# Kernel optimization log

Measured on AMD Instinct MI355X. Metric: run time of the kernel, lower is better.

## Reference

```python
import jax, jax.numpy as jnp
import numpy as np

N_NODES = 50000
N_EDGES = 600000
IN_DIM = 64
D = 128
N_LAYERS = 8
N_ETYPES = 44
N_MENTIONS = 100000
N_VARS = 20000
OUT_DIM = 100


def setup_inputs() -> dict:
    key = jax.random.key(0)
    ks = jax.random.split(key, 20)
    inp = {
        "node_labels": jax.random.normal(ks[0], (N_NODES, IN_DIM), jnp.float32),
        "edges": jax.random.randint(ks[1], (2, N_EDGES), 0, N_NODES, jnp.int32),
        "edge_labels": jax.random.randint(ks[2], (N_EDGES,), 0, N_ETYPES, jnp.int32),
        "var_gather": jax.random.randint(ks[3], (N_MENTIONS,), 0, N_NODES, jnp.int32),
        "var_scatter": jax.random.randint(ks[4], (N_MENTIONS,), 0, N_VARS, jnp.int32),
        "labels": jax.random.randint(ks[5], (N_VARS,), 0, OUT_DIM, jnp.int32),
        "num_vars": N_VARS,
    }
    s = 1.0 / np.sqrt(D)
    # node label encoder (2 layers)
    inp["enc_W0"] = jax.random.normal(ks[6], (IN_DIM, D), jnp.float32) / np.sqrt(IN_DIM)
    inp["enc_b0"] = jnp.zeros((D,), jnp.float32)
    inp["enc_W1"] = jax.random.normal(ks[7], (D, D), jnp.float32) * s
    inp["enc_b1"] = jnp.zeros((D,), jnp.float32)
    # 8 GGNN layers, stacked
    inp["edge_emb"] = jax.random.normal(ks[8], (N_LAYERS, N_ETYPES, D), jnp.float32) * s
    inp["mlp_W1"] = jax.random.normal(ks[9], (N_LAYERS, 3 * D, 2 * D), jnp.float32) / np.sqrt(3 * D)
    inp["mlp_b1"] = jnp.zeros((N_LAYERS, 2 * D), jnp.float32)
    inp["mlp_W2"] = jax.random.normal(ks[10], (N_LAYERS, 2 * D, D), jnp.float32) / np.sqrt(2 * D)
    inp["mlp_b2"] = jnp.zeros((N_LAYERS, D), jnp.float32)
    # independent type decoder (2 layers)
    inp["dec_W0"] = jax.random.normal(ks[11], (D, D), jnp.float32) * s
    inp["dec_b0"] = jnp.zeros((D,), jnp.float32)
    inp["dec_Wl"] = jax.random.normal(ks[12], (D, OUT_DIM), jnp.float32) * s
    inp["dec_bl"] = jnp.zeros((OUT_DIM,), jnp.float32)
    return inp


def reference(node_labels, edges, edge_labels, var_gather, var_scatter, labels, num_vars,
              enc_W0, enc_b0, enc_W1, enc_b1,
              edge_emb, mlp_W1, mlp_b1, mlp_W2, mlp_b2,
              dec_W0, dec_b0, dec_Wl, dec_bl):
    n_nodes = node_labels.shape[0]
    src, dst = edges[0], edges[1]  # message flows src -> dst (x_j = src, x_i = dst)

    # node label encoder
    h = node_labels @ enc_W0 + enc_b0
    h = jax.nn.relu(h) @ enc_W1 + enc_b1

    # message passing layers
    for l in range(edge_emb.shape[0]):
        ef = edge_emb[l][edge_labels]                       # [E, D]
        m = jnp.concatenate([h[dst], h[src], ef], axis=-1)  # [E, 3D]
        m = jax.nn.relu(m @ mlp_W1[l] + mlp_b1[l]) @ mlp_W2[l] + mlp_b2[l]
        h = jax.ops.segment_sum(m, dst, num_segments=n_nodes)
        h = jax.nn.gelu(h, approximate=False)  # torch nn.GELU (exact erf)

    # readout: gather variable mentions, scatter-mean into variables
    node_repr = h[var_gather]  # [M, D]
    sums = jax.ops.segment_sum(node_repr, var_scatter, num_segments=num_vars)
    counts = jax.ops.segment_sum(jnp.ones_like(var_scatter, jnp.float32), var_scatter, num_segments=num_vars)
    var_repr = sums / jnp.maximum(counts, 1.0)[:, None]

    # independent type decoder
    y = jax.nn.relu(var_repr @ dec_W0 + dec_b0)
    y = y @ dec_Wl + dec_bl
    return y
```

## Files before the change

### kernel.cpp

```cpp
#include <hip/hip_runtime.h>
#include <math.h>

#define N_NODES 50000
#define N_EDGES 600000
#define IN_DIM 64
#define DMODEL 128
#define N_LAYERS 8
#define N_ETYPES 44
#define N_MENTIONS 100000
#define N_VARS 20000
#define OUT_DIM 100

#define EPI_BIAS 0
#define EPI_BIAS_RELU 1
#define EPI_DEG_GELU 2
#define EPI_NONE 3

#define SCL  6.103515625e-05f
#define SCLI 16384.0f

typedef _Float16 f16x8 __attribute__((ext_vector_type(8)));
typedef _Float16 f16x4 __attribute__((ext_vector_type(4)));
typedef float f32x4 __attribute__((ext_vector_type(4)));

__device__ __forceinline__ float gelu_exact(float x) {
    return 0.5f * x * (1.0f + erff(x * 0.70710678118654752f));
}

__global__ void wprep(const float* __restrict__ src, _Float16* __restrict__ dhi,
                      _Float16* __restrict__ dlo, int K, int Nsrc, int Npad,
                      long srcLS, long dstLS, int cat) {
    __shared__ float sh[16][17];
    int z = blockIdx.z;
    src += (size_t)z * srcLS;
    dhi += (size_t)z * dstLS;
    dlo += (size_t)z * dstLS;
    int n0 = blockIdx.x * 16, k0 = blockIdx.y * 16;
    int tx = threadIdx.x, ty = threadIdx.y;
    int nr = n0 + tx, kr = k0 + ty;
    float v;
    if (cat) {
        int half = nr >> 8;
        int nc = nr & 255;
        v = src[(size_t)(kr + half * 128) * 256 + nc];
    } else {
        v = (nr < Nsrc) ? src[(size_t)kr * Nsrc + nr] : 0.f;
    }
    sh[ty][tx] = v;
    __syncthreads();
    float x = sh[tx][ty];
    int n = n0 + ty, k = k0 + tx;
    _Float16 hi = (_Float16)x;
    float lo = x - (float)hi;
    dhi[(size_t)n * K + k] = hi;
    dlo[(size_t)n * K + k] = (_Float16)lo;
}

template<int EPI, int ASPLIT, int OSPLIT, int MSWZ = 0, int NX = 8>
__global__ __launch_bounds__(256) void gemm3h(
        const float* __restrict__ A, const _Float16* __restrict__ Ahi,
        const _Float16* __restrict__ Alo,
        const _Float16* __restrict__ Bh, const _Float16* __restrict__ Bl,
        const float* __restrict__ bias, const int* __restrict__ deg,
        float* __restrict__ C, _Float16* __restrict__ Chi, _Float16* __restrict__ Clo,
        int M, int N, int K, int ldC) {
    __shared__ _Float16 Ah[64 * 56], Al[64 * 56], Bsh[64 * 56], Bsl[64 * 56];
    int t = threadIdx.x;
    int m0, n0;
    if (MSWZ) {
        int mpanels = (M + 63) >> 6;
        int per = (mpanels + 7) >> 3;
        int mi = blockIdx.x * per + blockIdx.y / NX;
        if (mi >= mpanels) return;
        m0 = mi * 64;
        n0 = (blockIdx.y % NX) * 64;
    } else {
        m0 = blockIdx.y * 64;
        n0 = blockIdx.x * 64;
    }
    int ar = t >> 2, ac = (t & 3) * 8;
    int btt = t & 127, br = btt >> 1, bc = (btt & 1) * 16;
    const _Float16* Bsrc = (t < 128) ? Bh : Bl;
    _Float16* Bdst = (t < 128) ? Bsh : Bsl;
    int lane = t & 63, wid = t >> 6;
    int wm = (wid >> 1) * 32, wn = (wid & 1) * 32;
    int quad = lane >> 4, l15 = lane & 15;
    f32x4 acc[2][2] = {};
    bool arow_ok = (m0 + ar) < M;
    const float* Aptr = ASPLIT ? nullptr : (A + (size_t)(m0 + ar) * K + ac);
    const _Float16* Ahp = ASPLIT ? (Ahi + (size_t)(m0 + ar) * K + ac) : nullptr;
    const _Float16* Alp = ASPLIT ? (Alo + (size_t)(m0 + ar) * K + ac) : nullptr;
    const _Float16* Bptr = Bsrc + (size_t)(n0 + br) * K + bc;

    for (int k0 = 0; k0 < K; k0 += 32) {
        f16x8 hv = {}, lv = {};
        if (ASPLIT) {
            if (arow_ok) {
                hv = *(const f16x8*)(Ahp + k0);
                lv = *(const f16x8*)(Alp + k0);
            }
        } else {
            float4 v0 = {0, 0, 0, 0}, v1 = {0, 0, 0, 0};
            if (arow_ok) {
                v0 = *(const float4*)(Aptr + k0);
                v1 = *(const float4*)(Aptr + k0 + 4);
            }
            float xs[8] = {v0.x, v0.y, v0.z, v0.w, v1.x, v1.y, v1.z, v1.w};
#pragma unroll
            for (int j = 0; j < 8; j++) {
                float s = xs[j] * SCL;
                _Float16 h = (_Float16)s;
                hv[j] = h;
                lv[j] = (_Float16)(s - (float)h);
            }
        }
        *(f16x8*)&Ah[ar * 56 + ac] = hv;
        *(f16x8*)&Al[ar * 56 + ac] = lv;
        f16x8 b0 = *(const f16x8*)(Bptr + k0);
        f16x8 b1v = *(const f16x8*)(Bptr + k0 + 8);
        *(f16x8*)&Bdst[br * 56 + bc] = b0;
        *(f16x8*)&Bdst[br * 56 + bc + 8] = b1v;
        __syncthreads();

        f16x8 afh[2], afl[2], bfh[2], bfl[2];
#pragma unroll
        for (int i = 0; i < 2; i++) {
            int am = (wm + i * 16 + l15) * 56 + quad * 8;
            afh[i] = *(const f16x8*)&Ah[am];
            afl[i] = *(const f16x8*)&Al[am];
            int bn = (wn + i * 16 + l15) * 56 + quad * 8;
            bfh[i] = *(const f16x8*)&Bsh[bn];
            bfl[i] = *(const f16x8*)&Bsl[bn];
        }
#pragma unroll
        for (int i = 0; i < 2; i++)
#pragma unroll
            for (int j = 0; j < 2; j++) {
                acc[i][j] = __builtin_amdgcn_mfma_f32_16x16x32_f16(afh[i], bfh[j], acc[i][j], 0, 0, 0);
                acc[i][j] = __builtin_amdgcn_mfma_f32_16x16x32_f16(afh[i], bfl[j], acc[i][j], 0, 0, 0);
                acc[i][j] = __builtin_amdgcn_mfma_f32_16x16x32_f16(afl[i], bfh[j], acc[i][j], 0, 0, 0);
            }
        __syncthreads();
    }

#pragma unroll
    for (int i = 0; i < 2; i++) {
        int rowb = m0 + wm + i * 16 + quad * 4;
#pragma unroll
        for (int j = 0; j < 2; j++) {
            int col = n0 + wn + j * 16 + l15;
            if (col >= N) continue;
#pragma unroll
            for (int r = 0; r < 4; r++) {
                int row = rowb + r;
                if (row >= M) continue;
                float v = acc[i][j][r] * SCLI;
                if (EPI == EPI_BIAS) { v += bias[col]; }
                else if (EPI == EPI_BIAS_RELU) { v += bias[col]; v = fmaxf(v, 0.f); }
                else if (EPI == EPI_DEG_GELU) { v += (float)deg[row] * bias[col]; v = gelu_exact(v); }
                if (OSPLIT == 0) {
                    C[(size_t)row * ldC + col] = v;
                } else if (OSPLIT == 1) {
                    float s = v * SCL;
                    _Float16 h = (_Float16)s;
                    size_t idx = (size_t)row * ldC + col;
                    Chi[idx] = h;
                    Clo[idx] = (_Float16)(s - (float)h);
                } else if (OSPLIT == 3) {
                    if (col < 256) C[(size_t)row * 256 + col] = v;
                    else Chi[(size_t)row * 256 + (col - 256)] = (_Float16)(v * SCL);
                }
            }
        }
    }
}

__global__ void count_deg(const int* __restrict__ dst, int* __restrict__ deg) {
    int e = blockIdx.x * blockDim.x + threadIdx.x;
    if (e < N_EDGES) atomicAdd(&deg[dst[e]], 1);
}

#define SCAN_B 1024
#define SCAN_NB ((N_NODES + SCAN_B - 1) / SCAN_B)

__global__ void scan_local(const int* __restrict__ deg, int* __restrict__ offs,
                           int* __restrict__ bsum, int n) {
    __shared__ int sh[SCAN_B];
    int t = threadIdx.x;
    int i = blockIdx.x * SCAN_B + t;
    int v = (i < n) ? deg[i] : 0;
    sh[t] = v;
    __syncthreads();
    for (int o = 1; o < SCAN_B; o <<= 1) {
        int u = (t >= o) ? sh[t - o] : 0;
        __syncthreads();
        sh[t] += u;
        __syncthreads();
    }
    if (i < n) offs[i] = sh[t] - v;
    if (t == SCAN_B - 1) bsum[blockIdx.x] = sh[t];
}

__global__ void scan_block(int* __restrict__ bsum, int nb) {
    __shared__ int sh[64];
    int t = threadIdx.x;
    int v = (t < nb) ? bsum[t] : 0;
    sh[t] = v;
    __syncthreads();
    for (int o = 1; o < 64; o <<= 1) {
        int u = (t >= o) ? sh[t - o] : 0;
        __syncthreads();
        sh[t] += u;
        __syncthreads();
    }
    if (t < nb) bsum[t] = sh[t] - v;
}

__global__ void scan_final(int* __restrict__ offs, const int* __restrict__ bsum,
                           int* __restrict__ cursor, int n, int total) {
    int i = blockIdx.x * SCAN_B + threadIdx.x;
    if (i < n) {
        int o = offs[i] + bsum[blockIdx.x];
        offs[i] = o;
        cursor[i] = o;
    }
    if (i == n) offs[n] = total;
}

__global__ void place_edges(const int* __restrict__ src, const int* __restrict__ dst,
                            const int* __restrict__ lab, int* __restrict__ cursor,
                            int* __restrict__ src_s, int* __restrict__ lab_s) {
    int e = blockIdx.x * blockDim.x + threadIdx.x;
    if (e < N_EDGES) {
        int pos = atomicAdd(&cursor[dst[e]], 1);
        src_s[pos] = src[e];
        lab_s[pos] = lab[e];
    }
}

__global__ void etype_proj_all(const float* __restrict__ edge_emb, const float* __restrict__ mlp_W1,
                               const float* __restrict__ mlp_b1, float* __restrict__ etp_all) {
    int et = blockIdx.x;
    int l  = blockIdx.y;
    int c = threadIdx.x;
    const float* ee = edge_emb + (size_t)l * N_ETYPES * DMODEL + (size_t)et * DMODEL;
    const float* W  = mlp_W1 + (size_t)l * 384 * 256 + (size_t)256 * 256;
    float s = mlp_b1[(size_t)l * 256 + c];
    for (int k = 0; k < DMODEL; k++)
        s += ee[k] * W[(size_t)k * 256 + c];
    etp_all[((size_t)l * N_ETYPES + et) * 256 + c] = s * SCL;
}

__global__ __launch_bounds__(256) void edge_agg(
        const float* __restrict__ HHd, const _Float16* __restrict__ HHs,
        const float* __restrict__ etp,
        const int* __restrict__ offsets, const int* __restrict__ src_s,
        const int* __restrict__ lab_s, _Float16* __restrict__ Phi,
        _Float16* __restrict__ Plo) {
    int wid = threadIdx.x >> 6, tl = threadIdx.x & 63;
    int i = blockIdx.x * 4 + wid;
    if (i >= N_NODES) return;
    int c4 = tl * 4;
    float4 hd = *(const float4*)&HHd[(size_t)i * 256 + c4];
    float hdx = hd.x * SCL, hdy = hd.y * SCL, hdz = hd.z * SCL, hdw = hd.w * SCL;
    float4 acc = {0.f, 0.f, 0.f, 0.f};
    int e0 = offsets[i], e1 = offsets[i + 1];
    int e = e0;
    for (; e + 3 < e1; e += 4) {
        int s0 = src_s[e],     l0 = lab_s[e];
        int s1 = src_s[e + 1], l1 = lab_s[e + 1];
        int s2 = src_s[e + 2], l2 = lab_s[e + 2];
        int s3 = src_s[e + 3], l3 = lab_s[e + 3];
        f16x4 hs0 = *(const f16x4*)&HHs[(size_t)s0 * 256 + c4];
        f16x4 hs1 = *(const f16x4*)&HHs[(size_t)s1 * 256 + c4];
        f16x4 hs2 = *(const f16x4*)&HHs[(size_t)s2 * 256 + c4];
        f16x4 hs3 = *(const f16x4*)&HHs[(size_t)s3 * 256 + c4];
        float4 et0 = *(const float4*)&etp[l0 * 256 + c4];
        float4 et1 = *(const float4*)&etp[l1 * 256 + c4];
        float4 et2 = *(const float4*)&etp[l2 * 256 + c4];
        float4 et3 = *(const float4*)&etp[l3 * 256 + c4];
        acc.x += fmaxf(hdx + (float)hs0[0] + et0.x, 0.f) + fmaxf(hdx + (float)hs1[0] + et1.x, 0.f)
               + fmaxf(hdx + (float)hs2[0] + et2.x, 0.f) + fmaxf(hdx + (float)hs3[0] + et3.x, 0.f);
        acc.y += fmaxf(hdy + (float)hs0[1] + et0.y, 0.f) + fmaxf(hdy + (float)hs1[1] + et1.y, 0.f)
               + fmaxf(hdy + (float)hs2[1] + et2.y, 0.f) + fmaxf(hdy + (float)hs3[1] + et3.y, 0.f);
        acc.z += fmaxf(hdz + (float)hs0[2] + et0.z, 0.f) + fmaxf(hdz + (float)hs1[2] + et1.z, 0.f)
               + fmaxf(hdz + (float)hs2[2] + et2.z, 0.f) + fmaxf(hdz + (float)hs3[2] + et3.z, 0.f);
        acc.w += fmaxf(hdw + (float)hs0[3] + et0.w, 0.f) + fmaxf(hdw + (float)hs1[3] + et1.w, 0.f)
               + fmaxf(hdw + (float)hs2[3] + et2.w, 0.f) + fmaxf(hdw + (float)hs3[3] + et3.w, 0.f);
    }
    for (; e < e1; ++e) {
        int s0 = src_s[e], l0 = lab_s[e];
        f16x4 hs0 = *(const f16x4*)&HHs[(size_t)s0 * 256 + c4];
        float4 et0 = *(const float4*)&etp[l0 * 256 + c4];
        acc.x += fmaxf(hdx + (float)hs0[0] + et0.x, 0.f);
        acc.y += fmaxf(hdy + (float)hs0[1] + et0.y, 0.f);
        acc.z += fmaxf(hdz + (float)hs0[2] + et0.z, 0.f);
        acc.w += fmaxf(hdw + (float)hs0[3] + et0.w, 0.f);
    }
    float sv[4] = {acc.x, acc.y, acc.z, acc.w};
    f16x4 ph, pl;
#pragma unroll
    for (int j = 0; j < 4; j++) {
        _Float16 h = (_Float16)sv[j];
        ph[j] = h;
        pl[j] = (_Float16)(sv[j] - (float)h);
    }
    *(f16x4*)&Phi[(size_t)i * 256 + c4] = ph;
    *(f16x4*)&Plo[(size_t)i * 256 + c4] = pl;
}

__global__ void readout_scatter(const _Float16* __restrict__ hhi, const _Float16* __restrict__ hlo,
                                const int* __restrict__ vg, const int* __restrict__ vs,
                                float* __restrict__ sums, int* __restrict__ cnt) {
    int m = blockIdx.x * 2 + (threadIdx.x >> 7);
    int c = threadIdx.x & 127;
    if (m >= N_MENTIONS) return;
    int node = vg[m];
    int v = vs[m];
    size_t idx = (size_t)node * DMODEL + c;
    float x = ((float)hhi[idx] + (float)hlo[idx]) * SCLI;
    atomicAdd(&sums[(size_t)v * DMODEL + c], x);
    if (c == 0) atomicAdd(&cnt[v], 1);
}

__global__ void divide_kernel(float* __restrict__ sums, const int* __restrict__ cnt) {
    int v = blockIdx.x;
    int c = threadIdx.x;
    float d = (float)max(cnt[v], 1);
    sums[(size_t)v * DMODEL + c] /= d;
}

extern "C" void kernel_launch(void* const* d_in, const int* in_sizes, int n_in,
                              void* d_out, int out_size, void* d_ws, size_t ws_size,
                              hipStream_t stream) {
    const float* node_labels = (const float*)d_in[0];
    const int*   edges       = (const int*)d_in[1];
    const int*   edge_labels = (const int*)d_in[2];
    const int*   var_gather  = (const int*)d_in[3];
    const int*   var_scatter = (const int*)d_in[4];
    const float* enc_W0 = (const float*)d_in[7];
    const float* enc_b0 = (const float*)d_in[8];
    const float* enc_W1 = (const float*)d_in[9];
    const float* enc_b1 = (const float*)d_in[10];
    const float* edge_emb = (const float*)d_in[11];
    const float* mlp_W1 = (const float*)d_in[12];
    const float* mlp_b1 = (const float*)d_in[13];
    const float* mlp_W2 = (const float*)d_in[14];
    const float* mlp_b2 = (const float*)d_in[15];
    const float* dec_W0 = (const float*)d_in[16];
    const float* dec_b0 = (const float*)d_in[17];
    const float* dec_Wl = (const float*)d_in[18];
    const float* dec_bl = (const float*)d_in[19];
    float* out = (float*)d_out;

    char* ws = (char*)d_ws;
    size_t off = 0;
    auto alloc = [&](size_t bytes) -> void* {
        void* p = ws + off;
        off += (bytes + 255) & ~(size_t)255;
        return p;
    };
    float*    HHd   = (float*)alloc((size_t)N_NODES * 256 * 4);
    _Float16* HHs   = (_Float16*)alloc((size_t)N_NODES * 256 * 2);
    _Float16* hhi   = (_Float16*)alloc((size_t)N_NODES * DMODEL * 2);
    _Float16* hlo   = (_Float16*)alloc((size_t)N_NODES * DMODEL * 2);
    _Float16* Phi   = (_Float16*)alloc((size_t)N_NODES * 256 * 2);
    _Float16* Plo   = (_Float16*)alloc((size_t)N_NODES * 256 * 2);
    float* etp_all = (float*)alloc((size_t)N_LAYERS * N_ETYPES * 256 * 4);
    int* deg    = (int*)alloc((size_t)N_NODES * 4);
    int* offs   = (int*)alloc((size_t)(N_NODES + 1) * 4);
    int* cursor = (int*)alloc((size_t)N_NODES * 4);
    int* bsum   = (int*)alloc(64 * 4);
    int* src_s  = (int*)alloc((size_t)N_EDGES * 4);
    int* lab_s  = (int*)alloc((size_t)N_EDGES * 4);
    _Float16* W1t_h = (_Float16*)alloc((size_t)N_LAYERS * 512 * 128 * 2);
    _Float16* W1t_l = (_Float16*)alloc((size_t)N_LAYERS * 512 * 128 * 2);
    _Float16* W2t_h = (_Float16*)alloc((size_t)N_LAYERS * 128 * 256 * 2);
    _Float16* W2t_l = (_Float16*)alloc((size_t)N_LAYERS * 128 * 256 * 2);
    _Float16* e0h = (_Float16*)alloc(128 * 64 * 2);
    _Float16* e0l = (_Float16*)alloc(128 * 64 * 2);
    _Float16* e1h = (_Float16*)alloc(128 * 128 * 2);
    _Float16* e1l = (_Float16*)alloc(128 * 128 * 2);
    _Float16* d0h = (_Float16*)alloc(128 * 128 * 2);
    _Float16* d0l = (_Float16*)alloc(128 * 128 * 2);
    _Float16* dlh = (_Float16*)alloc(128 * 128 * 2);
    _Float16* dll = (_Float16*)alloc(128 * 128 * 2);
    _Float16* hench = (_Float16*)alloc((size_t)N_NODES * DMODEL * 2);
    _Float16* hencl = (_Float16*)alloc((size_t)N_NODES * DMODEL * 2);
    float* vsum = (float*)alloc((size_t)N_VARS * DMODEL * 4);
    int*   vcnt = (int*)alloc((size_t)N_VARS * 4);
    _Float16* dtmph = (_Float16*)alloc((size_t)N_VARS * DMODEL * 2);
    _Float16* dtmpl = (_Float16*)alloc((size_t)N_VARS * DMODEL * 2);

    const int* e_src = edges;
    const int* e_dst = edges + N_EDGES;

    hipMemsetAsync(deg, 0, (size_t)N_NODES * 4, stream);
    hipMemsetAsync(vsum, 0, (size_t)N_VARS * DMODEL * 4, stream);
    hipMemsetAsync(vcnt, 0, (size_t)N_VARS * 4, stream);

    count_deg<<<(N_EDGES + 255) / 256, 256, 0, stream>>>(e_dst, deg);
    scan_local<<<SCAN_NB, SCAN_B, 0, stream>>>(deg, offs, bsum, N_NODES);
    scan_block<<<1, 64, 0, stream>>>(bsum, SCAN_NB);
    scan_final<<<SCAN_NB, SCAN_B, 0, stream>>>(offs, bsum, cursor, N_NODES, N_EDGES);
    place_edges<<<(N_EDGES + 255) / 256, 256, 0, stream>>>(e_src, e_dst, edge_labels, cursor,
                                                           src_s, lab_s);

    dim3 pb(16, 16);
    wprep<<<dim3(32, 8, N_LAYERS), pb, 0, stream>>>(mlp_W1, W1t_h, W1t_l, 128, 512, 512,
                                                    (long)384 * 256, (long)512 * 128, 1);
    wprep<<<dim3(8, 16, N_LAYERS), pb, 0, stream>>>(mlp_W2, W2t_h, W2t_l, 256, 128, 128,
                                                    (long)256 * 128, (long)128 * 256, 0);
    wprep<<<dim3(8, 4, 1), pb, 0, stream>>>(enc_W0, e0h, e0l, 64, 128, 128, 0, 0, 0);
    wprep<<<dim3(8, 8, 1), pb, 0, stream>>>(enc_W1, e1h, e1l, 128, 128, 128, 0, 0, 0);
    wprep<<<dim3(8, 8, 1), pb, 0, stream>>>(dec_W0, d0h, d0l, 128, 128, 128, 0, 0, 0);
    wprep<<<dim3(8, 8, 1), pb, 0, stream>>>(dec_Wl, dlh, dll, 128, 100, 128, 0, 0, 0);

    etype_proj_all<<<dim3(N_ETYPES, N_LAYERS), 256, 0, stream>>>(edge_emb, mlp_W1, mlp_b1, etp_all);

    dim3 blk(256);
    const int MT_N = (N_NODES + 63) / 64;
    const int MT_V = (N_VARS + 63) / 64;
    const int PER_N = (MT_N + 7) / 8;
    const int PER_V = (MT_V + 7) / 8;

    gemm3h<EPI_BIAS_RELU, 0, 1, 1, 2><<<dim3(8, PER_N * 2), blk, 0, stream>>>(
        node_labels, nullptr, nullptr, e0h, e0l, enc_b0, nullptr,
        nullptr, hench, hencl, N_NODES, 128, 64, 128);
    gemm3h<EPI_BIAS, 1, 1, 1, 2><<<dim3(8, PER_N * 2), blk, 0, stream>>>(
        nullptr, hench, hencl, e1h, e1l, enc_b1, nullptr,
        nullptr, hhi, hlo, N_NODES, 128, 128, 128);

    for (int l = 0; l < N_LAYERS; ++l) {
        const float* b2 = mlp_b2 + (size_t)l * DMODEL;
        gemm3h<EPI_NONE, 1, 3, 1, 8><<<dim3(8, PER_N * 8), blk, 0, stream>>>(
            nullptr, hhi, hlo, W1t_h + (size_t)l * 512 * 128, W1t_l + (size_t)l * 512 * 128,
            nullptr, nullptr, HHd, HHs, nullptr, N_NODES, 512, 128, 256);
        edge_agg<<<(N_NODES + 3) / 4, blk, 0, stream>>>(
            HHd, HHs, etp_all + (size_t)l * N_ETYPES * 256, offs, src_s, lab_s, Phi, Plo);
        gemm3h<EPI_DEG_GELU, 1, 1, 1, 2><<<dim3(8, PER_N * 2), blk, 0, stream>>>(
            nullptr, Phi, Plo, W2t_h + (size_t)l * 128 * 256, W2t_l + (size_t)l * 128 * 256,
            b2, deg, nullptr, hhi, hlo, N_NODES, 128, 256, 128);
    }

    readout_scatter<<<(N_MENTIONS + 1) / 2, 256, 0, stream>>>(hhi, hlo, var_gather, var_scatter,
                                                              vsum, vcnt);
    divide_kernel<<<N_VARS, DMODEL, 0, stream>>>(vsum, vcnt);

    gemm3h<EPI_BIAS_RELU, 0, 1, 1, 2><<<dim3(8, PER_V * 2), blk, 0, stream>>>(
        vsum, nullptr, nullptr, d0h, d0l, dec_b0, nullptr,
        nullptr, dtmph, dtmpl, N_VARS, 128, 128, 128);
    gemm3h<EPI_BIAS, 1, 0, 1, 2><<<dim3(8, PER_V * 2), blk, 0, stream>>>(
        nullptr, dtmph, dtmpl, dlh, dll, dec_bl, nullptr,
        out, nullptr, nullptr, N_VARS, OUT_DIM, 128, OUT_DIM);
}
```

Before: 1.308 ms.

## Add 128x128-tile split-fp16 GEMM kernel for per-layer MLP matmuls

Introduces a new gemm128 kernel using 128x128 output tiles with four waves each computing 64x64 via 16x16x32 fp16 MFMA, with three-term hi/lo split accumulation, and uses it for both per-layer node GEMMs. Larger tiles raise arithmetic intensity and reduce redundant global loads of A and B compared with the previous 64-row tiles. In exchange, the kernel uses more LDS (four 128x72 half buffers) and more accumulator registers, which may lower occupancy. It also drops the software pipelining the old kernel may have had, and the grid has fewer blocks.

```diff
diff --git a/kernel.cpp b/kernel.cpp
--- a/kernel.cpp
+++ b/kernel.cpp
@@ -161,6 +161,100 @@
                 if (OSPLIT == 0) {
                     C[(size_t)row * ldC + col] = v;
                 } else if (OSPLIT == 1) {
+                    float s = v * SCL;
+                    _Float16 h = (_Float16)s;
+                    size_t idx = (size_t)row * ldC + col;
+                    Chi[idx] = h;
+                    Clo[idx] = (_Float16)(s - (float)h);
+                } else if (OSPLIT == 3) {
+                    if (col < 256) C[(size_t)row * 256 + col] = v;
+                    else Chi[(size_t)row * 256 + (col - 256)] = (_Float16)(v * SCL);
+                }
+            }
+        }
+    }
+}
+
+#define PSTR 72
+
+template<int EPI, int OSPLIT, int NX>
+__global__ __launch_bounds__(256) void gemm128(
+        const _Float16* __restrict__ Ahi, const _Float16* __restrict__ Alo,
+        const _Float16* __restrict__ Bh, const _Float16* __restrict__ Bl,
+        const float* __restrict__ bias, const int* __restrict__ deg,
+        float* __restrict__ C, _Float16* __restrict__ Chi, _Float16* __restrict__ Clo,
+        int M, int K, int ldC) {
+    __shared__ _Float16 Ah[128 * PSTR], Al[128 * PSTR], Bsh[128 * PSTR], Bsl[128 * PSTR];
+    int t = threadIdx.x;
+    int mpanels = (M + 127) >> 7;
+    int per = (mpanels + 7) >> 3;
+    int mi = blockIdx.x * per + blockIdx.y / NX;
+    if (mi >= mpanels) return;
+    int m0 = mi * 128;
+    int n0 = (blockIdx.y % NX) * 128;
+    int lane = t & 63, wid = t >> 6;
+    int wm = (wid >> 1) * 64, wn = (wid & 1) * 64;
+    int quad = lane >> 4, l15 = lane & 15;
+    f32x4 acc[4][4] = {};
+
+    for (int k0 = 0; k0 < K; k0 += 64) {
+#pragma unroll
+        for (int i = 0; i < 4; ++i) {
+            int sid = t + 256 * i;
+            int r = sid >> 3, sg = sid & 7;
+            int ra = m0 + r;
+            if (ra > M - 1) ra = M - 1;
+            size_t ga = (size_t)ra * K + k0 + sg * 8;
+            size_t gb = (size_t)(n0 + r) * K + k0 + sg * 8;
+            f16x8 vh = *(const f16x8*)(Ahi + ga);
+            f16x8 vl = *(const f16x8*)(Alo + ga);
+            f16x8 wh = *(const f16x8*)(Bh + gb);
+            f16x8 wl = *(const f16x8*)(Bl + gb);
+            int lo = r * PSTR + sg * 8;
+            *(f16x8*)&Ah[lo] = vh;
+            *(f16x8*)&Al[lo] = vl;
+            *(f16x8*)&Bsh[lo] = wh;
+            *(f16x8*)&Bsl[lo] = wl;
+        }
+        __syncthreads();
+#pragma unroll
+        for (int ks = 0; ks < 2; ++ks) {
+            f16x8 ah[4], al[4], bh[4], bl[4];
+#pragma unroll
+            for (int f = 0; f < 4; ++f) {
+                int ao = (wm + f * 16 + l15) * PSTR + ks * 32 + quad * 8;
+                ah[f] = *(const f16x8*)&Ah[ao];
+                al[f] = *(const f16x8*)&Al[ao];
+                int bo = (wn + f * 16 + l15) * PSTR + ks * 32 + quad * 8;
+                bh[f] = *(const f16x8*)&Bsh[bo];
+                bl[f] = *(const f16x8*)&Bsl[bo];
+            }
+#pragma unroll
+            for (int fi = 0; fi < 4; ++fi)
+#pragma unroll
+                for (int fj = 0; fj < 4; ++fj) {
+                    acc[fi][fj] = __builtin_amdgcn_mfma_f32_16x16x32_f16(ah[fi], bh[fj], acc[fi][fj], 0, 0, 0);
+                    acc[fi][fj] = __builtin_amdgcn_mfma_f32_16x16x32_f16(ah[fi], bl[fj], acc[fi][fj], 0, 0, 0);
+                    acc[fi][fj] = __builtin_amdgcn_mfma_f32_16x16x32_f16(al[fi], bh[fj], acc[fi][fj], 0, 0, 0);
+                }
+        }
+        __syncthreads();
+    }
+
+#pragma unroll
+    for (int fi = 0; fi < 4; ++fi) {
+        int rowb = m0 + wm + fi * 16 + quad * 4;
+#pragma unroll
+        for (int fj = 0; fj < 4; ++fj) {
+            int col = n0 + wn + fj * 16 + l15;
+#pragma unroll
+            for (int r = 0; r < 4; ++r) {
+                int row = rowb + r;
+                if (row >= M) continue;
+                float v = acc[fi][fj][r] * SCLI;
+                if (EPI == EPI_BIAS) { v += bias[col]; }
+                else if (EPI == EPI_DEG_GELU) { v += (float)deg[row] * bias[col]; v = gelu_exact(v); }
+                if (OSPLIT == 1) {
                     float s = v * SCL;
                     _Float16 h = (_Float16)s;
                     size_t idx = (size_t)row * ldC + col;
@@ -423,6 +517,8 @@
     const int MT_V = (N_VARS + 63) / 64;
     const int PER_N = (MT_N + 7) / 8;
     const int PER_V = (MT_V + 7) / 8;
+    const int MP128 = (N_NODES + 127) / 128;
+    const int PER128 = (MP128 + 7) / 8;
 
     gemm3h<EPI_BIAS_RELU, 0, 1, 1, 2><<<dim3(8, PER_N * 2), blk, 0, stream>>>(
         node_labels, nullptr, nullptr, e0h, e0l, enc_b0, nullptr,
@@ -433,14 +529,14 @@
 
     for (int l = 0; l < N_LAYERS; ++l) {
         const float* b2 = mlp_b2 + (size_t)l * DMODEL;
-        gemm3h<EPI_NONE, 1, 3, 1, 8><<<dim3(8, PER_N * 8), blk, 0, stream>>>(
-            nullptr, hhi, hlo, W1t_h + (size_t)l * 512 * 128, W1t_l + (size_t)l * 512 * 128,
-            nullptr, nullptr, HHd, HHs, nullptr, N_NODES, 512, 128, 256);
+        gemm128<EPI_NONE, 3, 4><<<dim3(8, PER128 * 4), blk, 0, stream>>>(
+            hhi, hlo, W1t_h + (size_t)l * 512 * 128, W1t_l + (size_t)l * 512 * 128,
+            nullptr, nullptr, HHd, HHs, nullptr, N_NODES, 128, 256);
         edge_agg<<<(N_NODES + 3) / 4, blk, 0, stream>>>(
             HHd, HHs, etp_all + (size_t)l * N_ETYPES * 256, offs, src_s, lab_s, Phi, Plo);
-        gemm3h<EPI_DEG_GELU, 1, 1, 1, 2><<<dim3(8, PER_N * 2), blk, 0, stream>>>(
-            nullptr, Phi, Plo, W2t_h + (size_t)l * 128 * 256, W2t_l + (size_t)l * 128 * 256,
-            b2, deg, nullptr, hhi, hlo, N_NODES, 128, 256, 128);
+        gemm128<EPI_DEG_GELU, 1, 1><<<dim3(8, PER128), blk, 0, stream>>>(
+            Phi, Plo, W2t_h + (size_t)l * 128 * 256, W2t_l + (size_t)l * 128 * 256,
+            b2, deg, nullptr, hhi, hlo, N_NODES, 256, 128);
     }
 
     readout_scatter<<<(N_MENTIONS + 1) / 2, 256, 0, stream>>>(hhi, hlo, var_gather, var_scatter,
```

After: 1.365 ms. +4.4%, slower.
